# Optimization experiments

Measured on AMD Instinct MI355X. Metric: run time of the kernel, lower is better.

Reference implementation:

```python
import jax, jax.numpy as jnp
import numpy as np

N = 100000          # nodes
E = 1_600_000       # edges (nnz of sparse adj)
IN_F = 256
OUT_F = 128
DROP_P = 0.2


def setup_inputs() -> dict:
    key = jax.random.key(0)
    k1, k2, k3, k4, k5, k6 = jax.random.split(key, 6)
    return {
        "input": jax.random.normal(k1, (N, IN_F), dtype=jnp.float32),
        "weight": jax.random.normal(k2, (IN_F, OUT_F), dtype=jnp.float32) * 0.05,
        "adj_row": jax.random.randint(k3, (E,), 0, N, dtype=jnp.int32),
        "adj_col": jax.random.randint(k4, (E,), 0, N, dtype=jnp.int32),
        "adj_val": jax.random.uniform(k5, (E,), dtype=jnp.float32),
        "drop_u": jax.random.uniform(k6, (N, IN_F), dtype=jnp.float32),
    }


def reference(input, weight, adj_row, adj_col, adj_val, drop_u):
    # F.dropout(input, p, training=True): zero with prob p, scale survivors by 1/(1-p)
    x = jnp.where(drop_u > DROP_P, input / (1.0 - DROP_P), 0.0)
    # dense projection: [N, in] @ [in, out] -> [N, out]
    support = x @ weight
    # SpMM: out[r] = sum over edges e with row==r of val[e] * support[col[e]]
    gathered = support[adj_col] * adj_val[:, None]          # [E, out]
    output = jax.ops.segment_sum(gathered, adj_row, num_segments=N)  # [N, out]
    return output
```

## Files before the change

### kernel.cpp

```cpp
#include <hip/hip_runtime.h>

#define N_NODES 100000
#define IN_F 256
#define OUT_F 128
#define NB 782
#define CAP 2560
#define QCAP 896
#define TILE 4096

typedef __attribute__((ext_vector_type(8))) short v8s;
typedef __attribute__((ext_vector_type(4))) float v4f;

__device__ __forceinline__ unsigned short f2bf(float f) {
    unsigned int u = __float_as_uint(f);
    u += 0x7fffu + ((u >> 16) & 1u);
    return (unsigned short)(u >> 16);
}
__device__ __forceinline__ float bf2f(unsigned short s) {
    return __uint_as_float((unsigned int)s << 16);
}

__global__ void wt_kernel(const float* __restrict__ w, unsigned short* __restrict__ bt) {
    int idx = blockIdx.x * 256 + threadIdx.x;
    int k = idx >> 7;
    int n = idx & 127;
    bt[n * IN_F + k] = f2bf(w[idx]);
}

__global__ __launch_bounds__(256) void gemm_kernel(
    const float* __restrict__ x, const float* __restrict__ u,
    const unsigned short* __restrict__ bt, unsigned short* __restrict__ support) {
    const int tid  = threadIdx.x;
    const int lane = tid & 63;
    const int wv   = tid >> 6;
    const int cl   = lane & 15;
    const int kq   = lane >> 4;
    const long long row = (long long)blockIdx.x * 64 + wv * 16 + cl;
    const bool rv = row < N_NODES;
    const long long rowc = rv ? row : (N_NODES - 1);
    const float* xs = x + rowc * IN_F + kq * 8;
    const float* us = u + rowc * IN_F + kq * 8;
    const float m = rv ? 1.25f : 0.0f;
    const unsigned short* bb = bt + cl * IN_F + kq * 8;

    v4f acc[8] = {};
    float4 xa0A, xa1A, ua0A, ua1A, xa0B, xa1B, ua0B, ua1B;
    v8s bfA[8], bfB[8];

#define LA(s, X0, X1, U0, U1) \
    X0 = *(const float4*)(xs + (s) * 32); \
    X1 = *(const float4*)(xs + (s) * 32 + 4); \
    U0 = *(const float4*)(us + (s) * 32); \
    U1 = *(const float4*)(us + (s) * 32 + 4)

#define LB(s, BF) \
    _Pragma("unroll") \
    for (int tn = 0; tn < 8; ++tn) \
        BF[tn] = *(const v8s*)(bb + tn * 16 * IN_F + (s) * 32)

#define STEP(s, X0, X1, U0, U1, BF) \
    { \
        float4 x0 = X0, x1 = X1, u0 = U0, u1 = U1; \
        v8s bf[8]; \
        _Pragma("unroll") \
        for (int tn = 0; tn < 8; ++tn) bf[tn] = BF[tn]; \
        if ((s) < 6) { LA((s) + 2, X0, X1, U0, U1); LB((s) + 2, BF); } \
        unsigned short t0 = f2bf(u0.x > 0.2f ? x0.x * m : 0.0f); \
        unsigned short t1 = f2bf(u0.y > 0.2f ? x0.y * m : 0.0f); \
        unsigned short t2 = f2bf(u0.z > 0.2f ? x0.z * m : 0.0f); \
        unsigned short t3 = f2bf(u0.w > 0.2f ? x0.w * m : 0.0f); \
        unsigned short t4 = f2bf(u1.x > 0.2f ? x1.x * m : 0.0f); \
        unsigned short t5 = f2bf(u1.y > 0.2f ? x1.y * m : 0.0f); \
        unsigned short t6 = f2bf(u1.z > 0.2f ? x1.z * m : 0.0f); \
        unsigned short t7 = f2bf(u1.w > 0.2f ? x1.w * m : 0.0f); \
        v8s af = {(short)t0, (short)t1, (short)t2, (short)t3, \
                  (short)t4, (short)t5, (short)t6, (short)t7}; \
        _Pragma("unroll") \
        for (int tn = 0; tn < 8; ++tn) \
            acc[tn] = __builtin_amdgcn_mfma_f32_16x16x32_bf16(af, bf[tn], acc[tn], 0, 0, 0); \
    }

    LA(0, xa0A, xa1A, ua0A, ua1A); LB(0, bfA);
    LA(1, xa0B, xa1B, ua0B, ua1B); LB(1, bfB);

    STEP(0, xa0A, xa1A, ua0A, ua1A, bfA);
    STEP(1, xa0B, xa1B, ua0B, ua1B, bfB);
    STEP(2, xa0A, xa1A, ua0A, ua1A, bfA);
    STEP(3, xa0B, xa1B, ua0B, ua1B, bfB);
    STEP(4, xa0A, xa1A, ua0A, ua1A, bfA);
    STEP(5, xa0B, xa1B, ua0B, ua1B, bfB);
    STEP(6, xa0A, xa1A, ua0A, ua1A, bfA);
    STEP(7, xa0B, xa1B, ua0B, ua1B, bfB);

#undef LA
#undef LB
#undef STEP

    const int rq = lane >> 4;
    #pragma unroll
    for (int r = 0; r < 4; ++r) {
        long long g = (long long)blockIdx.x * 64 + wv * 16 + rq * 4 + r;
        if (g < N_NODES) {
            unsigned short* o = support + g * OUT_F + cl;
            #pragma unroll
            for (int tn = 0; tn < 8; ++tn)
                o[tn * 16] = f2bf(acc[tn][r]);
        }
    }
}

__global__ void init_kernel(int* __restrict__ cursor) {
    int i = blockIdx.x * 256 + threadIdx.x;
    if (i < NB) cursor[i * 16] = i * CAP;
}

__global__ __launch_bounds__(256) void scatter_kernel(
    const int* __restrict__ row, const int* __restrict__ col,
    const float* __restrict__ val, int* __restrict__ cursor,
    int2* __restrict__ cv, int E) {
    __shared__ int cnt[1024];
    __shared__ int loc[1024];
    __shared__ int delta[1024];
    __shared__ int tmp[256];
    __shared__ int gd[TILE];
    __shared__ int2 stage[TILE];
    __shared__ int total_s;
    const int tid = threadIdx.x;
    const int base_e = blockIdx.x * TILE;

    for (int i = tid; i < 1024; i += 256) cnt[i] = 0;
    __syncthreads();
    #pragma unroll
    for (int j = 0; j < TILE / 256; ++j) {
        int e = base_e + j * 256 + tid;
        if (e < E) atomicAdd(&cnt[row[e] >> 7], 1);
    }
    __syncthreads();
    int c0 = cnt[4*tid], c1 = cnt[4*tid+1], c2 = cnt[4*tid+2], c3 = cnt[4*tid+3];
    int s = c0 + c1 + c2 + c3;
    tmp[tid] = s;
    __syncthreads();
    #pragma unroll
    for (int d = 1; d < 256; d <<= 1) {
        int t = (tid >= d) ? tmp[tid - d] : 0;
        __syncthreads();
        tmp[tid] += t;
        __syncthreads();
    }
    int excl = tmp[tid] - s;
    loc[4*tid]   = excl;
    loc[4*tid+1] = excl + c0;
    loc[4*tid+2] = excl + c0 + c1;
    loc[4*tid+3] = excl + c0 + c1 + c2;
    if (tid == 255) total_s = tmp[255];
    __syncthreads();
    for (int i = tid; i < NB; i += 256) {
        int c = cnt[i];
        int gbase = 0;
        if (c > 0) gbase = atomicAdd(&cursor[i * 16], c);
        delta[i] = gbase - loc[i];
        cnt[i] = loc[i];
    }
    __syncthreads();
    #pragma unroll
    for (int j = 0; j < TILE / 256; ++j) {
        int e = base_e + j * 256 + tid;
        if (e < E) {
            int r = row[e];
            int b = r >> 7;
            int rank = atomicAdd(&cnt[b], 1);
            stage[rank] = make_int2(col[e] | ((r & 127) << 17), __float_as_int(val[e]));
            gd[rank] = delta[b] + rank;
        }
    }
    __syncthreads();
    int total = total_s;
    for (int i = tid; i < total; i += 256)
        cv[gd[i]] = stage[i];
}

__global__ __launch_bounds__(256) void acc2_kernel(
    const int* __restrict__ cursor, const int2* __restrict__ cv,
    const unsigned short* __restrict__ support, float* __restrict__ out) {
    __shared__ int2 sorted[QCAP];
    __shared__ int cnt_s[32];
    __shared__ int start_s[32];
    __shared__ int pos_s[32];
    const int tid = threadIdx.x;
    const int bq = blockIdx.x;
    const int b = bq >> 2;
    const int q = bq & 3;
    const int e0 = b * CAP;
    const int nE = cursor[b * 16] - e0;

    if (tid < 32) cnt_s[tid] = 0;
    __syncthreads();
    int2 ej[10];
    int  vj[10];
    #pragma unroll
    for (int j = 0; j < 10; ++j) {
        int i = j * 256 + tid;
        int2 c = cv[e0 + i];
        int lr = (c.x >> 17) & 127;
        int mine = (i < nE) && ((lr >> 5) == q);
        ej[j] = c;
        vj[j] = mine ? (lr & 31) : -1;
        if (mine) atomicAdd(&cnt_s[lr & 31], 1);
    }
    __syncthreads();
    if (tid < 32) {
        int v = cnt_s[tid];
        int sc = v;
        #pragma unroll
        for (int d = 1; d < 32; d <<= 1) {
            int t = __shfl_up(sc, d, 64);
            if (tid >= d) sc += t;
        }
        start_s[tid] = sc - v;
        pos_s[tid] = sc - v;
    }
    __syncthreads();
    #pragma unroll
    for (int j = 0; j < 10; ++j) {
        if (vj[j] >= 0) {
            int rank = atomicAdd(&pos_s[vj[j]], 1);
            sorted[rank] = ej[j];
        }
    }
    __syncthreads();
    const int lane = tid & 63, w = tid >> 6;
    const long long rowbase = (long long)b * 128 + q * 32;
    for (int rr = 0; rr < 8; ++rr) {
        int rl = w * 8 + rr;
        int e = start_s[rl];
        int end = e + cnt_s[rl];
        float a0 = 0.f, a1 = 0.f;
        for (; e < end; e += 8) {
            #pragma unroll
            for (int j = 0; j < 8; ++j) {
                int idx = e + j;
                int ids = min(idx, end - 1);
                int2 c = sorted[ids];
                float vv = (idx < end) ? __int_as_float(c.y) : 0.0f;
                int colv = c.x & 131071;
                unsigned int uu = *(const unsigned int*)(support + colv * OUT_F + lane * 2);
                a0 = fmaf(vv, bf2f((unsigned short)(uu & 0xffff)), a0);
                a1 = fmaf(vv, bf2f((unsigned short)(uu >> 16)), a1);
            }
        }
        long long g = rowbase + rl;
        if (g < N_NODES)
            *(float2*)(out + g * OUT_F + lane * 2) = make_float2(a0, a1);
    }
}

extern "C" void kernel_launch(void* const* d_in, const int* in_sizes, int n_in,
                              void* d_out, int out_size, void* d_ws, size_t ws_size,
                              hipStream_t stream) {
    const float* input   = (const float*)d_in[0];
    const float* weight  = (const float*)d_in[1];
    const int*   adj_row = (const int*)d_in[2];
    const int*   adj_col = (const int*)d_in[3];
    const float* adj_val = (const float*)d_in[4];
    const float* drop_u  = (const float*)d_in[5];
    float* out = (float*)d_out;
    const int E = in_sizes[2];

    char* p = (char*)d_ws;
    unsigned short* bt      = (unsigned short*)p;  p += 65536;
    int2*           cv      = (int2*)p;            p += (size_t)NB * CAP * sizeof(int2);
    unsigned short* support = (unsigned short*)p;  p += (size_t)N_NODES * OUT_F * 2;
    int*            cursor  = (int*)p;

    init_kernel<<<4, 256, 0, stream>>>(cursor);
    wt_kernel<<<128, 256, 0, stream>>>(weight, bt);
    gemm_kernel<<<(N_NODES + 63) / 64, 256, 0, stream>>>(input, drop_u, bt, support);
    scatter_kernel<<<(E + TILE - 1) / TILE, 256, 0, stream>>>(adj_row, adj_col, adj_val, cursor, cv, E);
    acc2_kernel<<<NB * 4, 256, 0, stream>>>(cursor, cv, support, out);
}
```

Before: 401.5 us.

## Stage dropout-masked A tile in LDS and pre-swizzle weights for coalesced loads

The GEMM now loads x and the dropout mask with fully coalesced float4 reads across the block, converts them to bf16 and stores them in a padded shared-memory tile. Each wave then reads its A fragments from LDS. The weight transpose kernel writes B in an MFMA-fragment-swizzled order so each lane reads contiguous 16-byte chunks. The loop is reorganized to iterate over output column tiles with a double-buffered B, which frees accumulator registers. In exchange this adds an LDS allocation (about 33KB per block), a barrier, and an extra LDS pass, which may reduce occupancy.

```diff
diff --git a/kernel.cpp b/kernel.cpp
--- a/kernel.cpp
+++ b/kernel.cpp
@@ -7,6 +7,7 @@
 #define CAP 2560
 #define QCAP 896
 #define TILE 4096
+#define ASTR 264
 
 typedef __attribute__((ext_vector_type(8))) short v8s;
 typedef __attribute__((ext_vector_type(4))) float v4f;
@@ -22,91 +23,80 @@
 
 __global__ void wt_kernel(const float* __restrict__ w, unsigned short* __restrict__ bt) {
     int idx = blockIdx.x * 256 + threadIdx.x;
-    int k = idx >> 7;
-    int n = idx & 127;
-    bt[n * IN_F + k] = f2bf(w[idx]);
+    int k   = idx >> 7;
+    int col = idx & 127;
+    int tn = col >> 4, cl = col & 15;
+    int s = k >> 5, kq = (k >> 3) & 3, i = k & 7;
+    bt[((tn * 8 + s) * 64 + kq * 16 + cl) * 8 + i] = f2bf(w[idx]);
 }
 
 __global__ __launch_bounds__(256) void gemm_kernel(
     const float* __restrict__ x, const float* __restrict__ u,
     const unsigned short* __restrict__ bt, unsigned short* __restrict__ support) {
+    __shared__ unsigned short As[64 * ASTR];
     const int tid  = threadIdx.x;
     const int lane = tid & 63;
     const int wv   = tid >> 6;
     const int cl   = lane & 15;
     const int kq   = lane >> 4;
-    const long long row = (long long)blockIdx.x * 64 + wv * 16 + cl;
-    const bool rv = row < N_NODES;
-    const long long rowc = rv ? row : (N_NODES - 1);
-    const float* xs = x + rowc * IN_F + kq * 8;
-    const float* us = u + rowc * IN_F + kq * 8;
-    const float m = rv ? 1.25f : 0.0f;
-    const unsigned short* bb = bt + cl * IN_F + kq * 8;
-
-    v4f acc[8] = {};
-    float4 xa0A, xa1A, ua0A, ua1A, xa0B, xa1B, ua0B, ua1B;
-    v8s bfA[8], bfB[8];
-
-#define LA(s, X0, X1, U0, U1) \
-    X0 = *(const float4*)(xs + (s) * 32); \
-    X1 = *(const float4*)(xs + (s) * 32 + 4); \
-    U0 = *(const float4*)(us + (s) * 32); \
-    U1 = *(const float4*)(us + (s) * 32 + 4)
-
-#define LB(s, BF) \
+    const long long base = (long long)blockIdx.x * 64;
+
+    {
+        const float4* x4 = (const float4*)(x + base * IN_F);
+        const float4* u4 = (const float4*)(u + base * IN_F);
+        const int fc = (tid & 63) * 4;
+        #pragma unroll
+        for (int j = 0; j < 16; ++j) {
+            const int row = j * 4 + (tid >> 6);
+            const bool ok = (base + row) < N_NODES;
+            float4 xi = ok ? x4[j * 256 + tid] : make_float4(0.f, 0.f, 0.f, 0.f);
+            float4 du = ok ? u4[j * 256 + tid] : make_float4(0.f, 0.f, 0.f, 0.f);
+            ushort4 pk;
+            pk.x = f2bf(du.x > 0.2f ? xi.x * 1.25f : 0.0f);
+            pk.y = f2bf(du.y > 0.2f ? xi.y * 1.25f : 0.0f);
+            pk.z = f2bf(du.z > 0.2f ? xi.z * 1.25f : 0.0f);
+            pk.w = f2bf(du.w > 0.2f ? xi.w * 1.25f : 0.0f);
+            *(ushort4*)(&As[row * ASTR + fc]) = pk;
+        }
+    }
+    __syncthreads();
+
+    v8s a[8];
+    #pragma unroll
+    for (int s = 0; s < 8; ++s)
+        a[s] = *(const v8s*)&As[(wv * 16 + cl) * ASTR + s * 32 + kq * 8];
+
+    const v8s* bp = (const v8s*)bt + lane;
+    const int rq = lane >> 4;
+    v8s bA[8], bB[8];
+    #pragma unroll
+    for (int s = 0; s < 8; ++s) bA[s] = bp[s * 64];
+
+#define PHASE(tn, BC, BN) { \
+    if ((tn) < 7) { \
+        _Pragma("unroll") \
+        for (int s = 0; s < 8; ++s) BN[s] = bp[((tn) + 1) * 512 + s * 64]; \
+    } \
+    v4f acc = {0.f, 0.f, 0.f, 0.f}; \
     _Pragma("unroll") \
-    for (int tn = 0; tn < 8; ++tn) \
-        BF[tn] = *(const v8s*)(bb + tn * 16 * IN_F + (s) * 32)
-
-#define STEP(s, X0, X1, U0, U1, BF) \
-    { \
-        float4 x0 = X0, x1 = X1, u0 = U0, u1 = U1; \
-        v8s bf[8]; \
-        _Pragma("unroll") \
-        for (int tn = 0; tn < 8; ++tn) bf[tn] = BF[tn]; \
-        if ((s) < 6) { LA((s) + 2, X0, X1, U0, U1); LB((s) + 2, BF); } \
-        unsigned short t0 = f2bf(u0.x > 0.2f ? x0.x * m : 0.0f); \
-        unsigned short t1 = f2bf(u0.y > 0.2f ? x0.y * m : 0.0f); \
-        unsigned short t2 = f2bf(u0.z > 0.2f ? x0.z * m : 0.0f); \
-        unsigned short t3 = f2bf(u0.w > 0.2f ? x0.w * m : 0.0f); \
-        unsigned short t4 = f2bf(u1.x > 0.2f ? x1.x * m : 0.0f); \
-        unsigned short t5 = f2bf(u1.y > 0.2f ? x1.y * m : 0.0f); \
-        unsigned short t6 = f2bf(u1.z > 0.2f ? x1.z * m : 0.0f); \
-        unsigned short t7 = f2bf(u1.w > 0.2f ? x1.w * m : 0.0f); \
-        v8s af = {(short)t0, (short)t1, (short)t2, (short)t3, \
-                  (short)t4, (short)t5, (short)t6, (short)t7}; \
-        _Pragma("unroll") \
-        for (int tn = 0; tn < 8; ++tn) \
-            acc[tn] = __builtin_amdgcn_mfma_f32_16x16x32_bf16(af, bf[tn], acc[tn], 0, 0, 0); \
-    }
-
-    LA(0, xa0A, xa1A, ua0A, ua1A); LB(0, bfA);
-    LA(1, xa0B, xa1B, ua0B, ua1B); LB(1, bfB);
-
-    STEP(0, xa0A, xa1A, ua0A, ua1A, bfA);
-    STEP(1, xa0B, xa1B, ua0B, ua1B, bfB);
-    STEP(2, xa0A, xa1A, ua0A, ua1A, bfA);
-    STEP(3, xa0B, xa1B, ua0B, ua1B, bfB);
-    STEP(4, xa0A, xa1A, ua0A, ua1A, bfA);
-    STEP(5, xa0B, xa1B, ua0B, ua1B, bfB);
-    STEP(6, xa0A, xa1A, ua0A, ua1A, bfA);
-    STEP(7, xa0B, xa1B, ua0B, ua1B, bfB);
-
-#undef LA
-#undef LB
-#undef STEP
-
-    const int rq = lane >> 4;
-    #pragma unroll
-    for (int r = 0; r < 4; ++r) {
-        long long g = (long long)blockIdx.x * 64 + wv * 16 + rq * 4 + r;
-        if (g < N_NODES) {
-            unsigned short* o = support + g * OUT_F + cl;
-            #pragma unroll
-            for (int tn = 0; tn < 8; ++tn)
-                o[tn * 16] = f2bf(acc[tn][r]);
-        }
-    }
+    for (int s = 0; s < 8; ++s) \
+        acc = __builtin_amdgcn_mfma_f32_16x16x32_bf16(a[s], BC[s], acc, 0, 0, 0); \
+    _Pragma("unroll") \
+    for (int r = 0; r < 4; ++r) { \
+        long long g = base + wv * 16 + rq * 4 + r; \
+        if (g < N_NODES) \
+            support[g * OUT_F + (tn) * 16 + cl] = f2bf(acc[r]); \
+    } }
+
+    PHASE(0, bA, bB)
+    PHASE(1, bB, bA)
+    PHASE(2, bA, bB)
+    PHASE(3, bB, bA)
+    PHASE(4, bA, bB)
+    PHASE(5, bB, bA)
+    PHASE(6, bA, bB)
+    PHASE(7, bB, bA)
+#undef PHASE
 }
 
 __global__ void init_kernel(int* __restrict__ cursor) {
```

Measured after the change: 373.7 us. 6.9% less time.
